# Performance work log

Measured on AMD Instinct MI355X. Metric: run time of the kernel, lower is better.

Reference implementation:

```python
import jax, jax.numpy as jnp
import numpy as np

HEADS = 8
DIM_HEAD = 64
SCALE = DIM_HEAD ** -0.5


def setup_inputs() -> dict:
    key = jax.random.key(0)
    ks = jax.random.split(key, 6)
    B, N, D = 1, 4096, 640
    INNER = HEADS * DIM_HEAD  # 512
    s = lambda fan_in: 1.0 / np.sqrt(fan_in)
    return {
        "x": jax.random.normal(ks[0], (B, N, D), dtype=jnp.float32),
        "Wq": jax.random.normal(ks[1], (D, INNER), dtype=jnp.float32) * s(D),
        "Wk": jax.random.normal(ks[2], (D, INNER), dtype=jnp.float32) * s(D),
        "Wv": jax.random.normal(ks[3], (D, INNER), dtype=jnp.float32) * s(D),
        "Wo": jax.random.normal(ks[4], (INNER, D), dtype=jnp.float32) * s(INNER),
        "bo": jnp.zeros((D,), dtype=jnp.float32),
    }


def reference(x, Wq, Wk, Wv, Wo, bo):
    B, N, _ = x.shape
    h, d = HEADS, DIM_HEAD
    # self-attention: context = x
    q = (x @ Wq).reshape(B, N, h, d).transpose(0, 2, 1, 3)  # [B,h,N,d]
    k = (x @ Wk).reshape(B, N, h, d).transpose(0, 2, 1, 3)
    v = (x @ Wv).reshape(B, N, h, d).transpose(0, 2, 1, 3)
    sim = jnp.einsum('bhid,bhjd->bhij', q, k) * SCALE  # [B,h,N,N]
    attn = jax.nn.softmax(sim, axis=-1)
    out = jnp.einsum('bhij,bhjd->bhid', attn, v)  # [B,h,N,d]
    out = out.transpose(0, 2, 1, 3).reshape(B, N, h * d)  # [B,N,inner]
    return out @ Wo + bo  # dropout p=0.0 is identity
```

## Files before the change

### kernel.cpp

```cpp
#include <hip/hip_runtime.h>
#include <math.h>

#define NSEQ   4096
#define DMODEL 640
#define NHEAD  8
#define DHEAD  64
#define INNER  512

typedef _Float16 f16;
typedef _Float16 f16x8 __attribute__((ext_vector_type(8)));
typedef _Float16 f16x4 __attribute__((ext_vector_type(4)));
typedef float    f32x4 __attribute__((ext_vector_type(4)));

#define MFMA16(a, b, c) __builtin_amdgcn_mfma_f32_16x16x32_f16((a), (b), (c), 0, 0, 0)

#define QSCALE 0.18033688011112042f

__device__ __forceinline__ void gl16(const f16* g, f16* l) {
    __builtin_amdgcn_global_load_lds(
        (const __attribute__((address_space(1))) unsigned int*)g,
        (__attribute__((address_space(3))) unsigned int*)l, 16, 0, 0);
}

__global__ __launch_bounds__(256) void cvt_x(const float* __restrict__ x,
                                             f16* __restrict__ xh) {
    int i = (blockIdx.x * 256 + threadIdx.x) * 8;
    float4 a = *(const float4*)&x[i];
    float4 b = *(const float4*)&x[i + 4];
    f16x8 o = {(f16)a.x, (f16)a.y, (f16)a.z, (f16)a.w,
               (f16)b.x, (f16)b.y, (f16)b.z, (f16)b.w};
    *(f16x8*)&xh[i] = o;
}

__global__ __launch_bounds__(256) void transpose_cvt3(
    const float* __restrict__ Wq, const float* __restrict__ Wk,
    const float* __restrict__ Wv,
    f16* __restrict__ WTq, f16* __restrict__ WTk, f16* __restrict__ WTv) {
    __shared__ __align__(16) f16 T[64][72];
    const float* src = blockIdx.z == 0 ? Wq : blockIdx.z == 1 ? Wk : Wv;
    f16* dst = blockIdx.z == 0 ? WTq : blockIdx.z == 1 ? WTk : WTv;
    const int R = DMODEL, C = INNER;
    const int c0 = blockIdx.x * 64, r0 = blockIdx.y * 64;
    const int t = threadIdx.x;
    {
        int r = t >> 2, cb = (t & 3) * 16;
#pragma unroll
        for (int i = 0; i < 16; i += 4) {
            float4 v = *(const float4*)&src[(size_t)(r0 + r) * C + c0 + cb + i];
            T[cb + i + 0][r] = (f16)v.x;
            T[cb + i + 1][r] = (f16)v.y;
            T[cb + i + 2][r] = (f16)v.z;
            T[cb + i + 3][r] = (f16)v.w;
        }
    }
    __syncthreads();
    {
        int c = t >> 2, rb = (t & 3) * 16;
        f16* d = dst + (size_t)(c0 + c) * R + r0 + rb;
        *(f16x8*)d = *(const f16x8*)&T[c][rb];
        *(f16x8*)(d + 8) = *(const f16x8*)&T[c][rb + 8];
    }
}

__global__ __launch_bounds__(256) void transpose_cvt(
    const float* __restrict__ src, f16* __restrict__ dst, int R, int C) {
    __shared__ __align__(16) f16 T[64][72];
    const int c0 = blockIdx.x * 64, r0 = blockIdx.y * 64;
    const int t = threadIdx.x;
    {
        int r = t >> 2, cb = (t & 3) * 16;
#pragma unroll
        for (int i = 0; i < 16; i += 4) {
            float4 v = *(const float4*)&src[(size_t)(r0 + r) * C + c0 + cb + i];
            T[cb + i + 0][r] = (f16)v.x;
            T[cb + i + 1][r] = (f16)v.y;
            T[cb + i + 2][r] = (f16)v.z;
            T[cb + i + 3][r] = (f16)v.w;
        }
    }
    __syncthreads();
    {
        int c = t >> 2, rb = (t & 3) * 16;
        f16* d = dst + (size_t)(c0 + c) * R + r0 + rb;
        *(f16x8*)d = *(const f16x8*)&T[c][rb];
        *(f16x8*)(d + 8) = *(const f16x8*)&T[c][rb + 8];
    }
}

__global__ __launch_bounds__(256) void qkv_gemm16(
    const f16* __restrict__ xh,
    const f16* __restrict__ WTq, const f16* __restrict__ WTk,
    const f16* __restrict__ WTv,
    f16* __restrict__ q16, f16* __restrict__ k16, f16* __restrict__ vT16)
{
    __shared__ __align__(16) f16 Xs[4096];
    __shared__ __align__(16) f16 Ws[4096];
    __shared__ __align__(16) f16 Cs[64][72];

    const int bx = blockIdx.x;
    const int by = blockIdx.y;
    const int bz = blockIdx.z;
    const f16* WT = (bz == 0) ? WTq : (bz == 1) ? WTk : WTv;

    const int tid = threadIdx.x;
    const int w = tid >> 6, lane = tid & 63;
    const int lr = lane & 15, lc = lane >> 4;
    const int srow8 = lane >> 3;
    const int le = 8 * ((lane & 7) ^ srow8);
    const int swz0 = 8 * (lc ^ (lr & 7));
    const int swz1 = 8 * ((lc + 4) ^ (lr & 7));
    const int m0 = by * 64, n0 = bx * 64;

    f32x4 acc[4] = {};

    for (int s = 0; s < DMODEL / 64; ++s) {
        const int k0 = s * 64;
#pragma unroll
        for (int c = 0; c < 2; ++c) {
            const int cc = w * 2 + c;
            gl16(xh + (size_t)(m0 + cc * 8 + srow8) * DMODEL + k0 + le,
                 &Xs[cc * 512]);
            gl16(WT + (size_t)(n0 + cc * 8 + srow8) * DMODEL + k0 + le,
                 &Ws[cc * 512]);
        }
        __syncthreads();
        f16x8 a0 = *(const f16x8*)&Xs[(16 * w + lr) * 64 + swz0];
        f16x8 a1 = *(const f16x8*)&Xs[(16 * w + lr) * 64 + swz1];
#pragma unroll
        for (int nt = 0; nt < 4; ++nt) {
            f16x8 b0 = *(const f16x8*)&Ws[(nt * 16 + lr) * 64 + swz0];
            f16x8 b1 = *(const f16x8*)&Ws[(nt * 16 + lr) * 64 + swz1];
            acc[nt] = MFMA16(a1, b1, MFMA16(a0, b0, acc[nt]));
        }
        __syncthreads();
    }

    const float sc = (bz == 0) ? QSCALE : 1.0f;
    if (bz < 2) {
#pragma unroll
        for (int nt = 0; nt < 4; ++nt)
#pragma unroll
            for (int r = 0; r < 4; ++r)
                Cs[16 * w + lc * 4 + r][nt * 16 + lr] = (f16)(acc[nt][r] * sc);
    } else {
#pragma unroll
        for (int nt = 0; nt < 4; ++nt)
#pragma unroll
            for (int r = 0; r < 4; ++r)
                Cs[nt * 16 + lr][16 * w + lc * 4 + r] = (f16)acc[nt][r];
    }
    __syncthreads();
    {
        const int rr = tid >> 2, cb = (tid & 3) * 16;
        f16x8 v0 = *(const f16x8*)&Cs[rr][cb];
        f16x8 v1 = *(const f16x8*)&Cs[rr][cb + 8];
        f16* dst;
        if (bz == 0)
            dst = q16 + ((size_t)bx * NSEQ + m0 + rr) * DHEAD + cb;
        else if (bz == 1)
            dst = k16 + ((size_t)bx * NSEQ + m0 + rr) * DHEAD + cb;
        else
            dst = vT16 + ((size_t)bx * DHEAD + rr) * NSEQ + m0 + cb;
        *(f16x8*)dst = v0;
        *(f16x8*)(dst + 8) = v1;
    }
}

__global__ __launch_bounds__(256, 4) void attn_fwd(
    const f16* __restrict__ q16, const f16* __restrict__ k16,
    const f16* __restrict__ vT16, f16* __restrict__ Opart,
    float* __restrict__ Ml)
{
    __shared__ __align__(16) f16 Ks[4096];
    __shared__ __align__(16) f16 Vt[4096];
    __shared__ __align__(16) f16 Ps[4096];

    const int lin = blockIdx.x + 64 * blockIdx.y + 512 * blockIdx.z;
    const int h  = lin & 7;
    const int qb = (lin >> 3) & 63;
    const int sp = lin >> 9;

    const int tid = threadIdx.x;
    const int w = tid >> 6, lane = tid & 63;
    const int lr = lane & 15, lc = lane >> 4;
    const int srow8 = lane >> 3;
    const int le = 8 * ((lane & 7) ^ srow8);
    const int swz0 = 8 * (lc ^ (lr & 7));
    const int swz1 = 8 * ((lc + 4) ^ (lr & 7));

    const f16* kp = k16 + ((size_t)h * NSEQ + sp * 2048) * DHEAD;
    const f16* vp = vT16 + (size_t)h * DHEAD * NSEQ + sp * 2048;

    const f16* qp = q16 + ((size_t)h * NSEQ + qb * 64 + 16 * w + lr) * DHEAD;
    const f16x8 qf0 = *(const f16x8*)&qp[lc * 8];
    const f16x8 qf1 = *(const f16x8*)&qp[32 + lc * 8];

    float m_run = -INFINITY, l_run = 0.f;
    f32x4 o[4] = {};

    for (int kt = 0; kt < 32; ++kt) {
#pragma unroll
        for (int c = 0; c < 2; ++c) {
            const int cc = 2 * w + c;
            gl16(kp + (size_t)(kt * 64 + cc * 8 + srow8) * DHEAD + le,
                 &Ks[cc * 512]);
            gl16(vp + (size_t)(cc * 8 + srow8) * NSEQ + kt * 64 + le,
                 &Vt[cc * 512]);
        }
        __syncthreads();

        f32x4 sv[4];
        const f32x4 z4 = {0.f, 0.f, 0.f, 0.f};
#pragma unroll
        for (int t = 0; t < 4; ++t) {
            f16x8 ka = *(const f16x8*)&Ks[(t * 16 + lr) * 64 + swz0];
            f16x8 kb = *(const f16x8*)&Ks[(t * 16 + lr) * 64 + swz1];
            sv[t] = MFMA16(kb, qf1, MFMA16(ka, qf0, z4));
        }

        float pm = sv[0][0];
#pragma unroll
        for (int t = 0; t < 4; ++t)
#pragma unroll
            for (int r = 0; r < 4; ++r) pm = fmaxf(pm, sv[t][r]);
        pm = fmaxf(pm, __shfl_xor(pm, 16));
        pm = fmaxf(pm, __shfl_xor(pm, 32));
        if (__any(pm > m_run)) {
            const float mn = fmaxf(m_run, pm);
            const float al = __builtin_amdgcn_exp2f(m_run - mn);
            m_run = mn;
            l_run *= al;
#pragma unroll
            for (int dt = 0; dt < 4; ++dt) o[dt] *= al;
        }
        float p[4][4];
        float ps = 0.f;
#pragma unroll
        for (int t = 0; t < 4; ++t)
#pragma unroll
            for (int r = 0; r < 4; ++r) {
                p[t][r] = __builtin_amdgcn_exp2f(sv[t][r] - m_run);
                ps += p[t][r];
            }
        ps += __shfl_xor(ps, 16);
        ps += __shfl_xor(ps, 32);
        l_run += ps;

#pragma unroll
        for (int t = 0; t < 4; ++t) {
            f16x4 pk = {(f16)p[t][0], (f16)p[t][1], (f16)p[t][2], (f16)p[t][3]};
            const int col = (16 * t + 4 * lc) ^ ((lr & 7) << 3);
            *(f16x4*)&Ps[(16 * w + lr) * 64 + col] = pk;
        }

        f16x8 pb0 = *(const f16x8*)&Ps[(16 * w + lr) * 64 + swz0];
        f16x8 pb1 = *(const f16x8*)&Ps[(16 * w + lr) * 64 + swz1];
#pragma unroll
        for (int dt = 0; dt < 4; ++dt) {
            f16x8 va0 = *(const f16x8*)&Vt[(dt * 16 + lr) * 64 + swz0];
            f16x8 va1 = *(const f16x8*)&Vt[(dt * 16 + lr) * 64 + swz1];
            o[dt] = MFMA16(va1, pb1, MFMA16(va0, pb0, o[dt]));
        }
        __syncthreads();
    }

    const float linv = 1.0f / l_run;
    const size_t qg = (size_t)qb * 64 + 16 * w + lr;
    f16* ob = Opart + (((size_t)(sp * 8 + h)) * NSEQ + qg) * DHEAD;
#pragma unroll
    for (int dt = 0; dt < 4; ++dt) {
        f16x4 ov = {(f16)(o[dt][0] * linv), (f16)(o[dt][1] * linv),
                    (f16)(o[dt][2] * linv), (f16)(o[dt][3] * linv)};
        *(f16x4*)&ob[dt * 16 + 4 * lc] = ov;
    }
    if (lc == 0) {
        float2 ml = make_float2(m_run, l_run);
        *(float2*)&Ml[(((size_t)(sp * 8 + h)) * NSEQ + qg) * 2] = ml;
    }
}

__global__ __launch_bounds__(256) void out_gemm16(
    const f16* __restrict__ Opart, const float* __restrict__ Ml,
    const f16* __restrict__ WoT,
    const float* __restrict__ bias, float* __restrict__ C)
{
    __shared__ __align__(16) f16 Xs[4096];
    __shared__ __align__(16) f16 Ws[4096];

    const int bx = blockIdx.x;
    const int by = blockIdx.y;
    const int tid = threadIdx.x;
    const int w = tid >> 6, lane = tid & 63;
    const int lr = lane & 15, lc = lane >> 4;
    const int srow8 = lane >> 3;
    const int j = lane & 7;
    const int le = 8 * (j ^ srow8);
    const int swz0 = 8 * (lc ^ (lr & 7));
    const int swz1 = 8 * ((lc + 4) ^ (lr & 7));
    const int m0 = by * 64, n0 = bx * 64;

    f32x4 acc[4] = {};

    for (int s8 = 0; s8 < 8; ++s8) {
        const int k0 = s8 * 64;
#pragma unroll
        for (int c = 0; c < 2; ++c) {
            const int cc = w * 2 + c;
            gl16(WoT + (size_t)(n0 + cc * 8 + srow8) * INNER + k0 + le,
                 &Ws[cc * 512]);
            const int row = cc * 8 + srow8;
            const size_t q = (size_t)m0 + row;
            f16x8 o0 = *(const f16x8*)&Opart[((size_t)s8 * NSEQ + q) * DHEAD + 8 * j];
            f16x8 o1 = *(const f16x8*)&Opart[((size_t)(8 + s8) * NSEQ + q) * DHEAD + 8 * j];
            float2 ml0 = *(const float2*)&Ml[((size_t)s8 * NSEQ + q) * 2];
            float2 ml1 = *(const float2*)&Ml[((size_t)(8 + s8) * NSEQ + q) * 2];
            const float mx = fmaxf(ml0.x, ml1.x);
            float w0 = ml0.y * __builtin_amdgcn_exp2f(ml0.x - mx);
            float w1 = ml1.y * __builtin_amdgcn_exp2f(ml1.x - mx);
            const float inv = 1.0f / (w0 + w1);
            w0 *= inv; w1 *= inv;
            f16x8 a8;
#pragma unroll
            for (int e = 0; e < 8; ++e)
                a8[e] = (f16)((float)o0[e] * w0 + (float)o1[e] * w1);
            *(f16x8*)&Xs[row * 64 + 8 * (j ^ (row & 7))] = a8;
        }
        __syncthreads();
        f16x8 a0 = *(const f16x8*)&Xs[(16 * w + lr) * 64 + swz0];
        f16x8 a1 = *(const f16x8*)&Xs[(16 * w + lr) * 64 + swz1];
#pragma unroll
        for (int nt = 0; nt < 4; ++nt) {
            f16x8 b0 = *(const f16x8*)&Ws[(nt * 16 + lr) * 64 + swz0];
            f16x8 b1 = *(const f16x8*)&Ws[(nt * 16 + lr) * 64 + swz1];
            acc[nt] = MFMA16(a1, b1, MFMA16(a0, b0, acc[nt]));
        }
        __syncthreads();
    }

#pragma unroll
    for (int nt = 0; nt < 4; ++nt) {
        const float b = bias[n0 + nt * 16 + lr];
#pragma unroll
        for (int r = 0; r < 4; ++r)
            C[(size_t)(m0 + 16 * w + lc * 4 + r) * DMODEL + n0 + nt * 16 + lr] =
                acc[nt][r] + b;
    }
}

extern "C" void kernel_launch(void* const* d_in, const int* in_sizes, int n_in,
                              void* d_out, int out_size, void* d_ws, size_t ws_size,
                              hipStream_t stream) {
    const float* x  = (const float*)d_in[0];
    const float* Wq = (const float*)d_in[1];
    const float* Wk = (const float*)d_in[2];
    const float* Wv = (const float*)d_in[3];
    const float* Wo = (const float*)d_in[4];
    const float* bo = (const float*)d_in[5];
    float* out = (float*)d_out;

    char* base = (char*)d_ws;
    f16*   Opart = (f16*)base;
    f16*   xh    = (f16*)base;
    f16*   WTq   = xh + (size_t)NSEQ * DMODEL;
    f16*   WTk   = WTq + (size_t)INNER * DMODEL;
    f16*   WTv   = WTk + (size_t)INNER * DMODEL;
    float* Ml    = (float*)(base + 8388608);
    f16*   WoT   = (f16*)(base + 8912896);
    f16*   q16   = (f16*)(base + 9568256);
    f16*   k16   = q16 + (size_t)NHEAD * NSEQ * DHEAD;
    f16*   vT16  = k16 + (size_t)NHEAD * NSEQ * DHEAD;

    cvt_x<<<NSEQ * DMODEL / (256 * 8), 256, 0, stream>>>(x, xh);
    transpose_cvt3<<<dim3(INNER / 64, DMODEL / 64, 3), 256, 0, stream>>>(
        Wq, Wk, Wv, WTq, WTk, WTv);
    transpose_cvt<<<dim3(DMODEL / 64, INNER / 64), 256, 0, stream>>>(
        Wo, WoT, INNER, DMODEL);

    qkv_gemm16<<<dim3(NHEAD, NSEQ / 64, 3), 256, 0, stream>>>(
        xh, WTq, WTk, WTv, q16, k16, vT16);
    attn_fwd<<<dim3(NSEQ / 64, NHEAD, 2), 256, 0, stream>>>(
        q16, k16, vT16, Opart, Ml);
    out_gemm16<<<dim3(DMODEL / 64, NSEQ / 64), 256, 0, stream>>>(
        Opart, Ml, WoT, bo, out);
}
```

Before: 171.5 us.

## Split KV four ways, reuse K tile for P, and widen QKV GEMM k-step

Attention now splits the key/value sequence into four chunks instead of two, which doubles the grid so more blocks are in flight. The P buffer is dropped by writing P into the K tile after an extra barrier, cutting shared memory so launch bounds can ask for 8 blocks per CU. The QKV GEMM now loads 128-wide k-slices per barrier to halve synchronisation. The output GEMM merges four partials, which costs more partial-output traffic, and the workspace offsets are enlarged to hold them.

Result: slower. 196.7 us (+14.7%).

```diff
diff --git a/kernel.cpp b/kernel.cpp
--- a/kernel.cpp
+++ b/kernel.cpp
@@ -6,6 +6,7 @@
 #define NHEAD  8
 #define DHEAD  64
 #define INNER  512
+#define KVSPLIT 4
 
 typedef _Float16 f16;
 typedef _Float16 f16x8 __attribute__((ext_vector_type(8)));
@@ -87,15 +88,15 @@
     }
 }
 
-__global__ __launch_bounds__(256) void qkv_gemm16(
+__global__ __launch_bounds__(256, 4) void qkv_gemm16(
     const f16* __restrict__ xh,
     const f16* __restrict__ WTq, const f16* __restrict__ WTk,
     const f16* __restrict__ WTv,
     f16* __restrict__ q16, f16* __restrict__ k16, f16* __restrict__ vT16)
 {
-    __shared__ __align__(16) f16 Xs[4096];
-    __shared__ __align__(16) f16 Ws[4096];
-    __shared__ __align__(16) f16 Cs[64][72];
+    __shared__ __align__(16) f16 Xs[8192];
+    __shared__ __align__(16) f16 Ws[8192];
+    f16 (*Cs)[72] = (f16(*)[72])Xs;
 
     const int bx = blockIdx.x;
     const int by = blockIdx.y;
@@ -113,24 +114,30 @@
 
     f32x4 acc[4] = {};
 
-    for (int s = 0; s < DMODEL / 64; ++s) {
-        const int k0 = s * 64;
-#pragma unroll
-        for (int c = 0; c < 2; ++c) {
-            const int cc = w * 2 + c;
-            gl16(xh + (size_t)(m0 + cc * 8 + srow8) * DMODEL + k0 + le,
-                 &Xs[cc * 512]);
-            gl16(WT + (size_t)(n0 + cc * 8 + srow8) * DMODEL + k0 + le,
-                 &Ws[cc * 512]);
-        }
-        __syncthreads();
-        f16x8 a0 = *(const f16x8*)&Xs[(16 * w + lr) * 64 + swz0];
-        f16x8 a1 = *(const f16x8*)&Xs[(16 * w + lr) * 64 + swz1];
-#pragma unroll
-        for (int nt = 0; nt < 4; ++nt) {
-            f16x8 b0 = *(const f16x8*)&Ws[(nt * 16 + lr) * 64 + swz0];
-            f16x8 b1 = *(const f16x8*)&Ws[(nt * 16 + lr) * 64 + swz1];
-            acc[nt] = MFMA16(a1, b1, MFMA16(a0, b0, acc[nt]));
+    for (int s = 0; s < DMODEL / 128; ++s) {
+        const int k0 = s * 128;
+#pragma unroll
+        for (int c = 0; c < 4; ++c) {
+            const int idx = w * 4 + c;
+            const int p = idx >> 3, cb = idx & 7;
+            gl16(xh + (size_t)(m0 + cb * 8 + srow8) * DMODEL + k0 + 64 * p + le,
+                 &Xs[p * 4096 + cb * 512]);
+            gl16(WT + (size_t)(n0 + cb * 8 + srow8) * DMODEL + k0 + 64 * p + le,
+                 &Ws[p * 4096 + cb * 512]);
+        }
+        __syncthreads();
+#pragma unroll
+        for (int ks = 0; ks < 2; ++ks) {
+            const f16* Xp = &Xs[ks * 4096];
+            const f16* Wp = &Ws[ks * 4096];
+            f16x8 a0 = *(const f16x8*)&Xp[(16 * w + lr) * 64 + swz0];
+            f16x8 a1 = *(const f16x8*)&Xp[(16 * w + lr) * 64 + swz1];
+#pragma unroll
+            for (int nt = 0; nt < 4; ++nt) {
+                f16x8 b0 = *(const f16x8*)&Wp[(nt * 16 + lr) * 64 + swz0];
+                f16x8 b1 = *(const f16x8*)&Wp[(nt * 16 + lr) * 64 + swz1];
+                acc[nt] = MFMA16(a1, b1, MFMA16(a0, b0, acc[nt]));
+            }
         }
         __syncthreads();
     }
@@ -166,14 +173,13 @@
     }
 }
 
-__global__ __launch_bounds__(256, 4) void attn_fwd(
+__global__ __launch_bounds__(256, 8) void attn_fwd(
     const f16* __restrict__ q16, const f16* __restrict__ k16,
     const f16* __restrict__ vT16, f16* __restrict__ Opart,
     float* __restrict__ Ml)
 {
     __shared__ __align__(16) f16 Ks[4096];
     __shared__ __align__(16) f16 Vt[4096];
-    __shared__ __align__(16) f16 Ps[4096];
 
     const int lin = blockIdx.x + 64 * blockIdx.y + 512 * blockIdx.z;
     const int h  = lin & 7;
@@ -188,8 +194,8 @@
     const int swz0 = 8 * (lc ^ (lr & 7));
     const int swz1 = 8 * ((lc + 4) ^ (lr & 7));
 
-    const f16* kp = k16 + ((size_t)h * NSEQ + sp * 2048) * DHEAD;
-    const f16* vp = vT16 + (size_t)h * DHEAD * NSEQ + sp * 2048;
+    const f16* kp = k16 + ((size_t)h * NSEQ + sp * (NSEQ / KVSPLIT)) * DHEAD;
+    const f16* vp = vT16 + (size_t)h * DHEAD * NSEQ + sp * (NSEQ / KVSPLIT);
 
     const f16* qp = q16 + ((size_t)h * NSEQ + qb * 64 + 16 * w + lr) * DHEAD;
     const f16x8 qf0 = *(const f16x8*)&qp[lc * 8];
@@ -198,7 +204,7 @@
     float m_run = -INFINITY, l_run = 0.f;
     f32x4 o[4] = {};
 
-    for (int kt = 0; kt < 32; ++kt) {
+    for (int kt = 0; kt < NSEQ / KVSPLIT / 64; ++kt) {
 #pragma unroll
         for (int c = 0; c < 2; ++c) {
             const int cc = 2 * w + c;
@@ -246,15 +252,17 @@
         ps += __shfl_xor(ps, 32);
         l_run += ps;
 
+        __syncthreads();
+
 #pragma unroll
         for (int t = 0; t < 4; ++t) {
             f16x4 pk = {(f16)p[t][0], (f16)p[t][1], (f16)p[t][2], (f16)p[t][3]};
             const int col = (16 * t + 4 * lc) ^ ((lr & 7) << 3);
-            *(f16x4*)&Ps[(16 * w + lr) * 64 + col] = pk;
-        }
-
-        f16x8 pb0 = *(const f16x8*)&Ps[(16 * w + lr) * 64 + swz0];
-        f16x8 pb1 = *(const f16x8*)&Ps[(16 * w + lr) * 64 + swz1];
+            *(f16x4*)&Ks[(16 * w + lr) * 64 + col] = pk;
+        }
+
+        f16x8 pb0 = *(const f16x8*)&Ks[(16 * w + lr) * 64 + swz0];
+        f16x8 pb1 = *(const f16x8*)&Ks[(16 * w + lr) * 64 + swz1];
 #pragma unroll
         for (int dt = 0; dt < 4; ++dt) {
             f16x8 va0 = *(const f16x8*)&Vt[(dt * 16 + lr) * 64 + swz0];
@@ -279,7 +287,7 @@
     }
 }
 
-__global__ __launch_bounds__(256) void out_gemm16(
+__global__ __launch_bounds__(256, 4) void out_gemm16(
     const f16* __restrict__ Opart, const float* __restrict__ Ml,
     const f16* __restrict__ WoT,
     const float* __restrict__ bias, float* __restrict__ C)
@@ -310,19 +318,33 @@
                  &Ws[cc * 512]);
             const int row = cc * 8 + srow8;
             const size_t q = (size_t)m0 + row;
-            f16x8 o0 = *(const f16x8*)&Opart[((size_t)s8 * NSEQ + q) * DHEAD + 8 * j];
-            f16x8 o1 = *(const f16x8*)&Opart[((size_t)(8 + s8) * NSEQ + q) * DHEAD + 8 * j];
-            float2 ml0 = *(const float2*)&Ml[((size_t)s8 * NSEQ + q) * 2];
-            float2 ml1 = *(const float2*)&Ml[((size_t)(8 + s8) * NSEQ + q) * 2];
-            const float mx = fmaxf(ml0.x, ml1.x);
-            float w0 = ml0.y * __builtin_amdgcn_exp2f(ml0.x - mx);
-            float w1 = ml1.y * __builtin_amdgcn_exp2f(ml1.x - mx);
-            const float inv = 1.0f / (w0 + w1);
-            w0 *= inv; w1 *= inv;
+            f16x8 op[KVSPLIT];
+            float mm[KVSPLIT], ll[KVSPLIT];
+#pragma unroll
+            for (int spp = 0; spp < KVSPLIT; ++spp) {
+                op[spp] = *(const f16x8*)
+                    &Opart[((size_t)(spp * 8 + s8) * NSEQ + q) * DHEAD + 8 * j];
+                float2 ml = *(const float2*)
+                    &Ml[((size_t)(spp * 8 + s8) * NSEQ + q) * 2];
+                mm[spp] = ml.x; ll[spp] = ml.y;
+            }
+            float mx = fmaxf(fmaxf(mm[0], mm[1]), fmaxf(mm[2], mm[3]));
+            float wt[KVSPLIT], tot = 0.f;
+#pragma unroll
+            for (int spp = 0; spp < KVSPLIT; ++spp) {
+                wt[spp] = ll[spp] * __builtin_amdgcn_exp2f(mm[spp] - mx);
+                tot += wt[spp];
+            }
+            const float inv = 1.0f / tot;
             f16x8 a8;
 #pragma unroll
-            for (int e = 0; e < 8; ++e)
-                a8[e] = (f16)((float)o0[e] * w0 + (float)o1[e] * w1);
+            for (int e = 0; e < 8; ++e) {
+                float v = 0.f;
+#pragma unroll
+                for (int spp = 0; spp < KVSPLIT; ++spp)
+                    v += (float)op[spp][e] * wt[spp];
+                a8[e] = (f16)(v * inv);
+            }
             *(f16x8*)&Xs[row * 64 + 8 * (j ^ (row & 7))] = a8;
         }
         __syncthreads();
@@ -364,9 +386,9 @@
     f16*   WTq   = xh + (size_t)NSEQ * DMODEL;
     f16*   WTk   = WTq + (size_t)INNER * DMODEL;
     f16*   WTv   = WTk + (size_t)INNER * DMODEL;
-    float* Ml    = (float*)(base + 8388608);
-    f16*   WoT   = (f16*)(base + 8912896);
-    f16*   q16   = (f16*)(base + 9568256);
+    float* Ml    = (float*)(base + 16777216);
+    f16*   WoT   = (f16*)(base + 17825792);
+    f16*   q16   = (f16*)(base + 18481152);
     f16*   k16   = q16 + (size_t)NHEAD * NSEQ * DHEAD;
     f16*   vT16  = k16 + (size_t)NHEAD * NSEQ * DHEAD;
 
@@ -378,7 +400,7 @@
 
     qkv_gemm16<<<dim3(NHEAD, NSEQ / 64, 3), 256, 0, stream>>>(
         xh, WTq, WTk, WTv, q16, k16, vT16);
-    attn_fwd<<<dim3(NSEQ / 64, NHEAD, 2), 256, 0, stream>>>(
+    attn_fwd<<<dim3(NSEQ / 64, NHEAD, KVSPLIT), 256, 0, stream>>>(
         q16, k16, vT16, Opart, Ml);
     out_gemm16<<<dim3(DMODEL / 64, NSEQ / 64), 256, 0, stream>>>(
         Opart, Ml, WoT, bo, out);
```

## Double-buffer K/V tiles and process 128 query rows per attention block

Applied to the files above, without the earlier changes.

The attention kernel now gives each wave two 16-row query groups, so a block covers 128 query rows and each K/V tile loaded into LDS is reused twice as often. K and V tiles are double-buffered: the next tile's global-to-LDS load is issued before computing on the current one, which removes one barrier per iteration and overlaps load latency with MFMA work. The cost is more registers and LDS, a lower occupancy target (launch bounds 2 instead of 4), and half as many blocks in the grid.

Result: no change. 172.6 us (+0.7%).

```diff
diff --git a/kernel.cpp b/kernel.cpp
--- a/kernel.cpp
+++ b/kernel.cpp
@@ -6,6 +6,7 @@
 #define NHEAD  8
 #define DHEAD  64
 #define INNER  512
+#define KVSPLIT 2
 
 typedef _Float16 f16;
 typedef _Float16 f16x8 __attribute__((ext_vector_type(8)));
@@ -166,19 +167,19 @@
     }
 }
 
-__global__ __launch_bounds__(256, 4) void attn_fwd(
+__global__ __launch_bounds__(256, 2) void attn_fwd(
     const f16* __restrict__ q16, const f16* __restrict__ k16,
     const f16* __restrict__ vT16, f16* __restrict__ Opart,
     float* __restrict__ Ml)
 {
-    __shared__ __align__(16) f16 Ks[4096];
-    __shared__ __align__(16) f16 Vt[4096];
-    __shared__ __align__(16) f16 Ps[4096];
-
-    const int lin = blockIdx.x + 64 * blockIdx.y + 512 * blockIdx.z;
+    __shared__ __align__(16) f16 KsB[2][4096];
+    __shared__ __align__(16) f16 VtB[2][4096];
+    __shared__ __align__(16) f16 Ps[8192];
+
+    const int lin = blockIdx.x + 32 * blockIdx.y + 256 * blockIdx.z;
     const int h  = lin & 7;
-    const int qb = (lin >> 3) & 63;
-    const int sp = lin >> 9;
+    const int qb = (lin >> 3) & 31;
+    const int sp = lin >> 8;
 
     const int tid = threadIdx.x;
     const int w = tid >> 6, lane = tid & 63;
@@ -188,94 +189,138 @@
     const int swz0 = 8 * (lc ^ (lr & 7));
     const int swz1 = 8 * ((lc + 4) ^ (lr & 7));
 
-    const f16* kp = k16 + ((size_t)h * NSEQ + sp * 2048) * DHEAD;
-    const f16* vp = vT16 + (size_t)h * DHEAD * NSEQ + sp * 2048;
-
-    const f16* qp = q16 + ((size_t)h * NSEQ + qb * 64 + 16 * w + lr) * DHEAD;
-    const f16x8 qf0 = *(const f16x8*)&qp[lc * 8];
-    const f16x8 qf1 = *(const f16x8*)&qp[32 + lc * 8];
-
-    float m_run = -INFINITY, l_run = 0.f;
-    f32x4 o[4] = {};
-
-    for (int kt = 0; kt < 32; ++kt) {
-#pragma unroll
-        for (int c = 0; c < 2; ++c) {
-            const int cc = 2 * w + c;
-            gl16(kp + (size_t)(kt * 64 + cc * 8 + srow8) * DHEAD + le,
-                 &Ks[cc * 512]);
-            gl16(vp + (size_t)(cc * 8 + srow8) * NSEQ + kt * 64 + le,
-                 &Vt[cc * 512]);
+    const f16* kp = k16 + ((size_t)h * NSEQ + sp * (NSEQ / KVSPLIT)) * DHEAD;
+    const f16* vp = vT16 + (size_t)h * DHEAD * NSEQ + sp * (NSEQ / KVSPLIT);
+
+    f16x8 qf[2][2];
+#pragma unroll
+    for (int g = 0; g < 2; ++g) {
+        const f16* qp = q16 +
+            ((size_t)h * NSEQ + qb * 128 + 32 * w + 16 * g + lr) * DHEAD;
+        qf[g][0] = *(const f16x8*)&qp[lc * 8];
+        qf[g][1] = *(const f16x8*)&qp[32 + lc * 8];
+    }
+
+    float m_run[2] = {-INFINITY, -INFINITY}, l_run[2] = {0.f, 0.f};
+    f32x4 o[2][4] = {};
+
+#pragma unroll
+    for (int c = 0; c < 2; ++c) {
+        const int cc = 2 * w + c;
+        gl16(kp + (size_t)(cc * 8 + srow8) * DHEAD + le, &KsB[0][cc * 512]);
+        gl16(vp + (size_t)(cc * 8 + srow8) * NSEQ + le, &VtB[0][cc * 512]);
+    }
+    __syncthreads();
+
+    const int NT = NSEQ / KVSPLIT / 64;
+    for (int kt = 0; kt < NT; ++kt) {
+        const int cur = kt & 1;
+        if (kt < NT - 1) {
+            const int nb = cur ^ 1;
+#pragma unroll
+            for (int c = 0; c < 2; ++c) {
+                const int cc = 2 * w + c;
+                gl16(kp + (size_t)((kt + 1) * 64 + cc * 8 + srow8) * DHEAD + le,
+                     &KsB[nb][cc * 512]);
+                gl16(vp + (size_t)(cc * 8 + srow8) * NSEQ + (kt + 1) * 64 + le,
+                     &VtB[nb][cc * 512]);
+            }
+        }
+
+        f32x4 s[2][4];
+        const f32x4 z4 = {0.f, 0.f, 0.f, 0.f};
+#pragma unroll
+        for (int t = 0; t < 4; ++t) {
+            f16x8 ka = *(const f16x8*)&KsB[cur][(t * 16 + lr) * 64 + swz0];
+            f16x8 kb = *(const f16x8*)&KsB[cur][(t * 16 + lr) * 64 + swz1];
+#pragma unroll
+            for (int g = 0; g < 2; ++g)
+                s[g][t] = MFMA16(kb, qf[g][1], MFMA16(ka, qf[g][0], z4));
+        }
+
+        float pm[2];
+#pragma unroll
+        for (int g = 0; g < 2; ++g) {
+            float m = s[g][0][0];
+#pragma unroll
+            for (int t = 0; t < 4; ++t)
+#pragma unroll
+                for (int r = 0; r < 4; ++r) m = fmaxf(m, s[g][t][r]);
+            m = fmaxf(m, __shfl_xor(m, 16));
+            m = fmaxf(m, __shfl_xor(m, 32));
+            pm[g] = m;
+        }
+        if (__any((pm[0] > m_run[0]) | (pm[1] > m_run[1]))) {
+#pragma unroll
+            for (int g = 0; g < 2; ++g) {
+                const float mn = fmaxf(m_run[g], pm[g]);
+                const float al = __builtin_amdgcn_exp2f(m_run[g] - mn);
+                m_run[g] = mn;
+                l_run[g] *= al;
+#pragma unroll
+                for (int dt = 0; dt < 4; ++dt) o[g][dt] *= al;
+            }
+        }
+#pragma unroll
+        for (int g = 0; g < 2; ++g) {
+            float ps = 0.f;
+#pragma unroll
+            for (int t = 0; t < 4; ++t)
+#pragma unroll
+                for (int r = 0; r < 4; ++r) {
+                    s[g][t][r] = __builtin_amdgcn_exp2f(s[g][t][r] - m_run[g]);
+                    ps += s[g][t][r];
+                }
+            ps += __shfl_xor(ps, 16);
+            ps += __shfl_xor(ps, 32);
+            l_run[g] += ps;
+        }
+
+#pragma unroll
+        for (int g = 0; g < 2; ++g) {
+            const int row = 32 * w + 16 * g + lr;
+#pragma unroll
+            for (int t = 0; t < 4; ++t) {
+                f16x4 pk = {(f16)s[g][t][0], (f16)s[g][t][1],
+                            (f16)s[g][t][2], (f16)s[g][t][3]};
+                const int col = (16 * t + 4 * lc) ^ ((lr & 7) << 3);
+                *(f16x4*)&Ps[row * 64 + col] = pk;
+            }
+        }
+
+        f16x8 pb[2][2];
+#pragma unroll
+        for (int g = 0; g < 2; ++g) {
+            const int row = 32 * w + 16 * g + lr;
+            pb[g][0] = *(const f16x8*)&Ps[row * 64 + swz0];
+            pb[g][1] = *(const f16x8*)&Ps[row * 64 + swz1];
+        }
+#pragma unroll
+        for (int dt = 0; dt < 4; ++dt) {
+            f16x8 va0 = *(const f16x8*)&VtB[cur][(dt * 16 + lr) * 64 + swz0];
+            f16x8 va1 = *(const f16x8*)&VtB[cur][(dt * 16 + lr) * 64 + swz1];
+#pragma unroll
+            for (int g = 0; g < 2; ++g)
+                o[g][dt] = MFMA16(va1, pb[g][1], MFMA16(va0, pb[g][0], o[g][dt]));
         }
         __syncthreads();
-
-        f32x4 sv[4];
-        const f32x4 z4 = {0.f, 0.f, 0.f, 0.f};
-#pragma unroll
-        for (int t = 0; t < 4; ++t) {
-            f16x8 ka = *(const f16x8*)&Ks[(t * 16 + lr) * 64 + swz0];
-            f16x8 kb = *(const f16x8*)&Ks[(t * 16 + lr) * 64 + swz1];
-            sv[t] = MFMA16(kb, qf1, MFMA16(ka, qf0, z4));
-        }
-
-        float pm = sv[0][0];
-#pragma unroll
-        for (int t = 0; t < 4; ++t)
-#pragma unroll
-            for (int r = 0; r < 4; ++r) pm = fmaxf(pm, sv[t][r]);
-        pm = fmaxf(pm, __shfl_xor(pm, 16));
-        pm = fmaxf(pm, __shfl_xor(pm, 32));
-        if (__any(pm > m_run)) {
-            const float mn = fmaxf(m_run, pm);
-            const float al = __builtin_amdgcn_exp2f(m_run - mn);
-            m_run = mn;
-            l_run *= al;
-#pragma unroll
-            for (int dt = 0; dt < 4; ++dt) o[dt] *= al;
-        }
-        float p[4][4];
-        float ps = 0.f;
-#pragma unroll
-        for (int t = 0; t < 4; ++t)
-#pragma unroll
-            for (int r = 0; r < 4; ++r) {
-                p[t][r] = __builtin_amdgcn_exp2f(sv[t][r] - m_run);
-                ps += p[t][r];
-            }
-        ps += __shfl_xor(ps, 16);
-        ps += __shfl_xor(ps, 32);
-        l_run += ps;
-
-#pragma unroll
-        for (int t = 0; t < 4; ++t) {
-            f16x4 pk = {(f16)p[t][0], (f16)p[t][1], (f16)p[t][2], (f16)p[t][3]};
-            const int col = (16 * t + 4 * lc) ^ ((lr & 7) << 3);
-            *(f16x4*)&Ps[(16 * w + lr) * 64 + col] = pk;
-        }
-
-        f16x8 pb0 = *(const f16x8*)&Ps[(16 * w + lr) * 64 + swz0];
-        f16x8 pb1 = *(const f16x8*)&Ps[(16 * w + lr) * 64 + swz1];
+    }
+
+#pragma unroll
+    for (int g = 0; g < 2; ++g) {
+        const float linv = 1.0f / l_run[g];
+        const size_t qg = (size_t)qb * 128 + 32 * w + 16 * g + lr;
+        f16* ob = Opart + (((size_t)(sp * 8 + h)) * NSEQ + qg) * DHEAD;
 #pragma unroll
         for (int dt = 0; dt < 4; ++dt) {
-            f16x8 va0 = *(const f16x8*)&Vt[(dt * 16 + lr) * 64 + swz0];
-            f16x8 va1 = *(const f16x8*)&Vt[(dt * 16 + lr) * 64 + swz1];
-            o[dt] = MFMA16(va1, pb1, MFMA16(va0, pb0, o[dt]));
-        }
-        __syncthreads();
-    }
-
-    const float linv = 1.0f / l_run;
-    const size_t qg = (size_t)qb * 64 + 16 * w + lr;
-    f16* ob = Opart + (((size_t)(sp * 8 + h)) * NSEQ + qg) * DHEAD;
-#pragma unroll
-    for (int dt = 0; dt < 4; ++dt) {
-        f16x4 ov = {(f16)(o[dt][0] * linv), (f16)(o[dt][1] * linv),
-                    (f16)(o[dt][2] * linv), (f16)(o[dt][3] * linv)};
-        *(f16x4*)&ob[dt * 16 + 4 * lc] = ov;
-    }
-    if (lc == 0) {
-        float2 ml = make_float2(m_run, l_run);
-        *(float2*)&Ml[(((size_t)(sp * 8 + h)) * NSEQ + qg) * 2] = ml;
+            f16x4 ov = {(f16)(o[g][dt][0] * linv), (f16)(o[g][dt][1] * linv),
+                        (f16)(o[g][dt][2] * linv), (f16)(o[g][dt][3] * linv)};
+            *(f16x4*)&ob[dt * 16 + 4 * lc] = ov;
+        }
+        if (lc == 0) {
+            float2 ml = make_float2(m_run[g], l_run[g]);
+            *(float2*)&Ml[(((size_t)(sp * 8 + h)) * NSEQ + qg) * 2] = ml;
+        }
     }
 }
 
@@ -378,7 +423,7 @@
 
     qkv_gemm16<<<dim3(NHEAD, NSEQ / 64, 3), 256, 0, stream>>>(
         xh, WTq, WTk, WTv, q16, k16, vT16);
-    attn_fwd<<<dim3(NSEQ / 64, NHEAD, 2), 256, 0, stream>>>(
+    attn_fwd<<<dim3(NSEQ / 128, NHEAD, KVSPLIT), 256, 0, stream>>>(
         q16, k16, vT16, Opart, Ml);
     out_gemm16<<<dim3(DMODEL / 64, NSEQ / 64), 256, 0, stream>>>(
         Opart, Ml, WoT, bo, out);
```
